# Optimization experiments

Measured on AMD Instinct MI355X. Metric: run time of the kernel, lower is better.

Reference implementation:

```python
import jax, jax.numpy as jnp
import numpy as np
import math

N = 400000  # total anchors across FPN levels
M = 128     # GT boxes per image
IOU_LOW, IOU_HIGH = 0.3, 0.6
SCALE_CLAMP = math.log(224.0 / 8.0)
NEUTRAL = -1.0e8


def setup_inputs() -> dict:
    key = jax.random.key(0)
    k1, k2, k3, k4, k5, k6 = jax.random.split(key, 6)
    # anchors: valid XYXY boxes centered in an 800x800 image
    ctr = jax.random.uniform(k1, (N, 2), minval=0.0, maxval=800.0)
    half = jax.random.uniform(k2, (N, 2), minval=8.0, maxval=64.0)
    anchors = jnp.concatenate([ctr - half, ctr + half], axis=1)
    deltas = jax.random.normal(k3, (N, 4)) * 0.2
    # GT boxes (M, 5): XYXY + class id
    gctr = jax.random.uniform(k4, (M, 2), minval=0.0, maxval=800.0)
    ghalf = jax.random.uniform(k5, (M, 2), minval=10.0, maxval=120.0)
    cls = jnp.floor(jax.random.uniform(k6, (M, 1), minval=0.0, maxval=20.0))
    gt_boxes = jnp.concatenate([gctr - ghalf, gctr + ghalf, cls], axis=1)
    return {"anchors": anchors, "deltas": deltas, "gt_boxes": gt_boxes}


def apply_deltas_to_anchors(deltas, anchors):
    # mirrors rcnn_apply_deltas_to_anchors (note: pw/ph are HALF widths/heights)
    dx = deltas[:, 0]
    dy = deltas[:, 1]
    dw = jnp.minimum(deltas[:, 2], SCALE_CLAMP)
    dh = jnp.minimum(deltas[:, 3], SCALE_CLAMP)
    px = (anchors[:, 0] + anchors[:, 2]) * 0.5
    py = (anchors[:, 1] + anchors[:, 3]) * 0.5
    pw = (anchors[:, 2] - anchors[:, 0]) * 0.5
    ph = (anchors[:, 3] - anchors[:, 1]) * 0.5
    bx = px + pw * dx
    by = py + ph * dy
    bw = pw * jnp.exp(dw)
    bh = ph * jnp.exp(dh)
    return jnp.stack([bx - bw, by - bh, bx + bw, by + bh], axis=-1)


def pairwise_iou(b1, b2):
    # (Nm, 4) x (Nn, 4) -> (Nm, Nn), XYXY format, mirrors iou()
    x1 = jnp.maximum(b1[:, None, 0], b2[None, :, 0])
    y1 = jnp.maximum(b1[:, None, 1], b2[None, :, 1])
    x2 = jnp.minimum(b1[:, None, 2], b2[None, :, 2])
    y2 = jnp.minimum(b1[:, None, 3], b2[None, :, 3])
    xl = x2 - x1
    yl = y2 - y1
    inter = jnp.where((xl > 0) & (yl > 0), xl * yl, 0.0)
    area1 = (b1[:, 2] - b1[:, 0]) * (b1[:, 3] - b1[:, 1])
    area2 = (b2[:, 2] - b2[:, 0]) * (b2[:, 3] - b2[:, 1])
    union = area1[:, None] + area2[None, :] - inter
    return inter / union


def reference(anchors, deltas, gt_boxes):
    proposals = apply_deltas_to_anchors(deltas, anchors)
    # 2) match anchors to GT (rcnn_match_anchors_to_gt).
    #    Invalid GT (class == -1) are masked out of the IoU matrix instead of
    #    filtered (keeps static shapes under jit).
    valid = gt_boxes[:, 4] != -1
    m = pairwise_iou(anchors, gt_boxes[:, :4])          # (N, M)
    m = jnp.where(valid[None, :], m, -1.0)
    match_quality = jnp.max(m, axis=1)                   # (N,)
    matched_idxs = jnp.argmax(m, axis=1)                 # (N,)
    matched_gt = gt_boxes[matched_idxs]                  # (N, 5)
    matched_gt = jnp.where((match_quality <= IOU_LOW)[:, None], -1.0, matched_gt)
    neutral = (match_quality > IOU_LOW) & (match_quality < IOU_HIGH)
    matched_gt = jnp.where(neutral[:, None], NEUTRAL, matched_gt)
    return proposals, matched_gt
```

## Files before the change

### kernel.cpp

```cpp
#include <hip/hip_runtime.h>
#include <math.h>

#define MAX_GT 128

__global__ __launch_bounds__(256) void rpn_match_kernel(
    const float* __restrict__ anchors,
    const float* __restrict__ deltas,
    const float* __restrict__ gt_boxes,
    float* __restrict__ out,
    int n, int m)
{
    __shared__ float4 sbox[MAX_GT];
    __shared__ float  sarea[MAX_GT];
    __shared__ float  scls[MAX_GT];

    const int tid = threadIdx.x;
    if (tid < m) {
        float g0 = gt_boxes[tid * 5 + 0];
        float g1 = gt_boxes[tid * 5 + 1];
        float g2 = gt_boxes[tid * 5 + 2];
        float g3 = gt_boxes[tid * 5 + 3];
        float g4 = gt_boxes[tid * 5 + 4];
        bool valid = (g4 != -1.0f);
        sbox[tid] = valid ? make_float4(g0, g1, g2, g3)
                          : make_float4(1e30f, 1e30f, -1e30f, -1e30f);
        sarea[tid] = valid ? (g2 - g0) * (g3 - g1) : 0.0f;
        scls[tid]  = g4;
    }
    __syncthreads();

    const int i0 = blockIdx.x * 512 + tid;
    const int i1 = i0 + 256;
    const bool v0 = (i0 < n);
    const bool v1 = (i1 < n);
    const int i0c = v0 ? i0 : 0;
    const int i1c = v1 ? i1 : 0;

    const float4 a0 = reinterpret_cast<const float4*>(anchors)[i0c];
    const float4 a1 = reinterpret_cast<const float4*>(anchors)[i1c];
    const float4 d0 = reinterpret_cast<const float4*>(deltas)[i0c];
    const float4 d1 = reinterpret_cast<const float4*>(deltas)[i1c];

    const float SCALE_CLAMP = 3.3322045101752038f;
    {
        float pw = (a0.z - a0.x) * 0.5f, ph = (a0.w - a0.y) * 0.5f;
        float px = (a0.x + a0.z) * 0.5f, py = (a0.y + a0.w) * 0.5f;
        float bx = px + pw * d0.x, by = py + ph * d0.y;
        float bw = pw * expf(fminf(d0.z, SCALE_CLAMP));
        float bh = ph * expf(fminf(d0.w, SCALE_CLAMP));
        if (v0) reinterpret_cast<float4*>(out)[i0] =
            make_float4(bx - bw, by - bh, bx + bw, by + bh);
    }
    {
        float pw = (a1.z - a1.x) * 0.5f, ph = (a1.w - a1.y) * 0.5f;
        float px = (a1.x + a1.z) * 0.5f, py = (a1.y + a1.w) * 0.5f;
        float bx = px + pw * d1.x, by = py + ph * d1.y;
        float bw = pw * expf(fminf(d1.z, SCALE_CLAMP));
        float bh = ph * expf(fminf(d1.w, SCALE_CLAMP));
        if (v1) reinterpret_cast<float4*>(out)[i1] =
            make_float4(bx - bw, by - bh, bx + bw, by + bh);
    }

    const float ar0 = (a0.z - a0.x) * (a0.w - a0.y);
    const float ar1 = (a1.z - a1.x) * (a1.w - a1.y);

    float4 b = sbox[0];
    float ga = sarea[0];
    float bI0, bS0, bI1, bS1;
    int bidx0 = 0, bidx1 = 0;
    {
        float xl = fminf(a0.z, b.z) - fmaxf(a0.x, b.x);
        float yl = fminf(a0.w, b.w) - fmaxf(a0.y, b.y);
        bI0 = fmaxf(xl, 0.0f) * fmaxf(yl, 0.0f);
        bS0 = ar0 + ga;
        xl = fminf(a1.z, b.z) - fmaxf(a1.x, b.x);
        yl = fminf(a1.w, b.w) - fmaxf(a1.y, b.y);
        bI1 = fmaxf(xl, 0.0f) * fmaxf(yl, 0.0f);
        bS1 = ar1 + ga;
    }

    #pragma unroll 8
    for (int j = 1; j < m; ++j) {
        b  = sbox[j];
        ga = sarea[j];
        {
            float xl = fminf(a0.z, b.z) - fmaxf(a0.x, b.x);
            float yl = fminf(a0.w, b.w) - fmaxf(a0.y, b.y);
            float inter = fmaxf(xl, 0.0f) * fmaxf(yl, 0.0f);
            float S = ar0 + ga;
            bool g = (inter * bS0) > (bI0 * S);
            bI0   = g ? inter : bI0;
            bS0   = g ? S     : bS0;
            bidx0 = g ? j     : bidx0;
        }
        {
            float xl = fminf(a1.z, b.z) - fmaxf(a1.x, b.x);
            float yl = fminf(a1.w, b.w) - fmaxf(a1.y, b.y);
            float inter = fmaxf(xl, 0.0f) * fmaxf(yl, 0.0f);
            float S = ar1 + ga;
            bool g = (inter * bS1) > (bI1 * S);
            bI1   = g ? inter : bI1;
            bS1   = g ? S     : bS1;
            bidx1 = g ? j     : bidx1;
        }
    }

    const float IOU_LOW = 0.3f, IOU_HIGH = 0.6f, NEUTRAL = -100000000.0f;
    float* mout = out + (size_t)n * 4;

    {
        float uni = bS0 - bI0;
        float q = bI0 / uni;
        float o0, o1, o2, o3, o4;
        if (q <= IOU_LOW) {
            o0 = o1 = o2 = o3 = o4 = -1.0f;
        } else if (q < IOU_HIGH) {
            o0 = o1 = o2 = o3 = o4 = NEUTRAL;
        } else {
            float4 gbx = sbox[bidx0];
            o0 = gbx.x; o1 = gbx.y; o2 = gbx.z; o3 = gbx.w; o4 = scls[bidx0];
        }
        if (v0) {
            float* mo = mout + (size_t)i0 * 5;
            mo[0] = o0; mo[1] = o1; mo[2] = o2; mo[3] = o3; mo[4] = o4;
        }
    }
    {
        float uni = bS1 - bI1;
        float q = bI1 / uni;
        float o0, o1, o2, o3, o4;
        if (q <= IOU_LOW) {
            o0 = o1 = o2 = o3 = o4 = -1.0f;
        } else if (q < IOU_HIGH) {
            o0 = o1 = o2 = o3 = o4 = NEUTRAL;
        } else {
            float4 gbx = sbox[bidx1];
            o0 = gbx.x; o1 = gbx.y; o2 = gbx.z; o3 = gbx.w; o4 = scls[bidx1];
        }
        if (v1) {
            float* mo = mout + (size_t)i1 * 5;
            mo[0] = o0; mo[1] = o1; mo[2] = o2; mo[3] = o3; mo[4] = o4;
        }
    }
}

extern "C" void kernel_launch(void* const* d_in, const int* in_sizes, int n_in,
                              void* d_out, int out_size, void* d_ws, size_t ws_size,
                              hipStream_t stream) {
    const float* anchors  = (const float*)d_in[0];
    const float* deltas   = (const float*)d_in[1];
    const float* gt_boxes = (const float*)d_in[2];
    float* out = (float*)d_out;

    int n = in_sizes[0] / 4;
    int m = in_sizes[2] / 5;

    int nblocks = (n + 511) / 512;
    hipLaunchKernelGGL(rpn_match_kernel, dim3(nblocks), dim3(256), 0, stream,
                       anchors, deltas, gt_boxes, out, n, m);
}
```

Baseline: 94.36 us.

## Precompute GT table in a prep kernel and read it via uniform global loads

Adds a separate one-block kernel that writes padded GT boxes, areas and classes to workspace, so the main kernel no longer fills shared memory or calls __syncthreads. In the loop, GT data is read from global memory at a block-uniform index, which the compiler can turn into scalar loads, and the two anchors' IoU math is packed into float2 vectors to encourage packed FP32 instructions. The cost is an extra kernel launch and dependence on scalar cache hits for the GT table.

```diff
diff --git a/kernel.cpp b/kernel.cpp
--- a/kernel.cpp
+++ b/kernel.cpp
@@ -1,34 +1,47 @@
 #include <hip/hip_runtime.h>
 #include <math.h>
 
-#define MAX_GT 128
+typedef float v2f __attribute__((ext_vector_type(2)));
+
+__device__ __forceinline__ v2f v2_min(v2f a, float b) {
+    v2f r; r.x = fminf(a.x, b); r.y = fminf(a.y, b); return r;
+}
+__device__ __forceinline__ v2f v2_max(v2f a, float b) {
+    v2f r; r.x = fmaxf(a.x, b); r.y = fmaxf(a.y, b); return r;
+}
+__device__ __forceinline__ v2f v2_max0(v2f a) {
+    v2f r; r.x = fmaxf(a.x, 0.0f); r.y = fmaxf(a.y, 0.0f); return r;
+}
+
+__global__ void prep_kernel(const float* __restrict__ gt, float* __restrict__ pre, int m) {
+    int j = threadIdx.x;
+    if (j < m) {
+        float g0 = gt[j * 5 + 0];
+        float g1 = gt[j * 5 + 1];
+        float g2 = gt[j * 5 + 2];
+        float g3 = gt[j * 5 + 3];
+        float g4 = gt[j * 5 + 4];
+        bool valid = (g4 != -1.0f);
+        float* p = pre + j * 8;
+        if (valid) {
+            p[0] = g0; p[1] = g1; p[2] = g2; p[3] = g3;
+            p[4] = (g2 - g0) * (g3 - g1);
+        } else {
+            p[0] = 1e30f; p[1] = 1e30f; p[2] = -1e30f; p[3] = -1e30f;
+            p[4] = 0.0f;
+        }
+        p[5] = g4; p[6] = 0.0f; p[7] = 0.0f;
+    }
+}
 
 __global__ __launch_bounds__(256) void rpn_match_kernel(
     const float* __restrict__ anchors,
     const float* __restrict__ deltas,
-    const float* __restrict__ gt_boxes,
+    const float* __restrict__ pre,
     float* __restrict__ out,
     int n, int m)
 {
-    __shared__ float4 sbox[MAX_GT];
-    __shared__ float  sarea[MAX_GT];
-    __shared__ float  scls[MAX_GT];
-
     const int tid = threadIdx.x;
-    if (tid < m) {
-        float g0 = gt_boxes[tid * 5 + 0];
-        float g1 = gt_boxes[tid * 5 + 1];
-        float g2 = gt_boxes[tid * 5 + 2];
-        float g3 = gt_boxes[tid * 5 + 3];
-        float g4 = gt_boxes[tid * 5 + 4];
-        bool valid = (g4 != -1.0f);
-        sbox[tid] = valid ? make_float4(g0, g1, g2, g3)
-                          : make_float4(1e30f, 1e30f, -1e30f, -1e30f);
-        sarea[tid] = valid ? (g2 - g0) * (g3 - g1) : 0.0f;
-        scls[tid]  = g4;
-    }
-    __syncthreads();
-
     const int i0 = blockIdx.x * 512 + tid;
     const int i1 = i0 + 256;
     const bool v0 = (i0 < n);
@@ -61,64 +74,61 @@
             make_float4(bx - bw, by - bh, bx + bw, by + bh);
     }
 
-    const float ar0 = (a0.z - a0.x) * (a0.w - a0.y);
-    const float ar1 = (a1.z - a1.x) * (a1.w - a1.y);
+    v2f ax; ax.x = a0.x; ax.y = a1.x;
+    v2f ay; ay.x = a0.y; ay.y = a1.y;
+    v2f az; az.x = a0.z; az.y = a1.z;
+    v2f aw; aw.x = a0.w; aw.y = a1.w;
+    v2f ar; ar.x = (a0.z - a0.x) * (a0.w - a0.y);
+            ar.y = (a1.z - a1.x) * (a1.w - a1.y);
 
-    float4 b = sbox[0];
-    float ga = sarea[0];
-    float bI0, bS0, bI1, bS1;
+    const float4* p4 = reinterpret_cast<const float4*>(pre);
+
+    v2f bI, bS;
     int bidx0 = 0, bidx1 = 0;
     {
-        float xl = fminf(a0.z, b.z) - fmaxf(a0.x, b.x);
-        float yl = fminf(a0.w, b.w) - fmaxf(a0.y, b.y);
-        bI0 = fmaxf(xl, 0.0f) * fmaxf(yl, 0.0f);
-        bS0 = ar0 + ga;
-        xl = fminf(a1.z, b.z) - fmaxf(a1.x, b.x);
-        yl = fminf(a1.w, b.w) - fmaxf(a1.y, b.y);
-        bI1 = fmaxf(xl, 0.0f) * fmaxf(yl, 0.0f);
-        bS1 = ar1 + ga;
+        float4 b = p4[0];
+        float ga = p4[1].x;
+        v2f xl = v2_min(az, b.z) - v2_max(ax, b.x);
+        v2f yl = v2_min(aw, b.w) - v2_max(ay, b.y);
+        bI = v2_max0(xl) * v2_max0(yl);
+        bS = ar + ga;
     }
 
     #pragma unroll 8
     for (int j = 1; j < m; ++j) {
-        b  = sbox[j];
-        ga = sarea[j];
-        {
-            float xl = fminf(a0.z, b.z) - fmaxf(a0.x, b.x);
-            float yl = fminf(a0.w, b.w) - fmaxf(a0.y, b.y);
-            float inter = fmaxf(xl, 0.0f) * fmaxf(yl, 0.0f);
-            float S = ar0 + ga;
-            bool g = (inter * bS0) > (bI0 * S);
-            bI0   = g ? inter : bI0;
-            bS0   = g ? S     : bS0;
-            bidx0 = g ? j     : bidx0;
-        }
-        {
-            float xl = fminf(a1.z, b.z) - fmaxf(a1.x, b.x);
-            float yl = fminf(a1.w, b.w) - fmaxf(a1.y, b.y);
-            float inter = fmaxf(xl, 0.0f) * fmaxf(yl, 0.0f);
-            float S = ar1 + ga;
-            bool g = (inter * bS1) > (bI1 * S);
-            bI1   = g ? inter : bI1;
-            bS1   = g ? S     : bS1;
-            bidx1 = g ? j     : bidx1;
-        }
+        float4 b  = p4[2 * j];
+        float  ga = p4[2 * j + 1].x;
+        v2f xl = v2_min(az, b.z) - v2_max(ax, b.x);
+        v2f yl = v2_min(aw, b.w) - v2_max(ay, b.y);
+        v2f inter = v2_max0(xl) * v2_max0(yl);
+        v2f S = ar + ga;
+        v2f lhs = inter * bS;
+        v2f rhs = bI * S;
+        bool g0 = lhs.x > rhs.x;
+        bool g1 = lhs.y > rhs.y;
+        bI.x  = g0 ? inter.x : bI.x;
+        bS.x  = g0 ? S.x     : bS.x;
+        bidx0 = g0 ? j       : bidx0;
+        bI.y  = g1 ? inter.y : bI.y;
+        bS.y  = g1 ? S.y     : bS.y;
+        bidx1 = g1 ? j       : bidx1;
     }
 
     const float IOU_LOW = 0.3f, IOU_HIGH = 0.6f, NEUTRAL = -100000000.0f;
     float* mout = out + (size_t)n * 4;
 
     {
-        float uni = bS0 - bI0;
-        float q = bI0 / uni;
+        float uni = bS.x - bI.x;
+        float q = bI.x / uni;
         float o0, o1, o2, o3, o4;
         if (q <= IOU_LOW) {
             o0 = o1 = o2 = o3 = o4 = -1.0f;
         } else if (q < IOU_HIGH) {
             o0 = o1 = o2 = o3 = o4 = NEUTRAL;
         } else {
-            float4 gbx = sbox[bidx0];
-            o0 = gbx.x; o1 = gbx.y; o2 = gbx.z; o3 = gbx.w; o4 = scls[bidx0];
+            float4 gbx = p4[2 * bidx0];
+            o0 = gbx.x; o1 = gbx.y; o2 = gbx.z; o3 = gbx.w;
+            o4 = p4[2 * bidx0 + 1].y;
         }
         if (v0) {
             float* mo = mout + (size_t)i0 * 5;
@@ -126,16 +136,17 @@
         }
     }
     {
-        float uni = bS1 - bI1;
-        float q = bI1 / uni;
+        float uni = bS.y - bI.y;
+        float q = bI.y / uni;
         float o0, o1, o2, o3, o4;
         if (q <= IOU_LOW) {
             o0 = o1 = o2 = o3 = o4 = -1.0f;
         } else if (q < IOU_HIGH) {
             o0 = o1 = o2 = o3 = o4 = NEUTRAL;
         } else {
-            float4 gbx = sbox[bidx1];
-            o0 = gbx.x; o1 = gbx.y; o2 = gbx.z; o3 = gbx.w; o4 = scls[bidx1];
+            float4 gbx = p4[2 * bidx1];
+            o0 = gbx.x; o1 = gbx.y; o2 = gbx.z; o3 = gbx.w;
+            o4 = p4[2 * bidx1 + 1].y;
         }
         if (v1) {
             float* mo = mout + (size_t)i1 * 5;
@@ -151,11 +162,14 @@
     const float* deltas   = (const float*)d_in[1];
     const float* gt_boxes = (const float*)d_in[2];
     float* out = (float*)d_out;
+    float* pre = (float*)d_ws;
 
     int n = in_sizes[0] / 4;
     int m = in_sizes[2] / 5;
 
+    hipLaunchKernelGGL(prep_kernel, dim3(1), dim3(256), 0, stream, gt_boxes, pre, m);
+
     int nblocks = (n + 511) / 512;
     hipLaunchKernelGGL(rpn_match_kernel, dim3(nblocks), dim3(256), 0, stream,
-                       anchors, deltas, gt_boxes, out, n, m);
+                       anchors, deltas, pre, out, n, m);
 }
```

Measured after the change: 99.55 us. 1.06x slower.
